# Optimization experiments

Hardware: AMD Instinct MI355X
Metric: run time of the kernel (lower is better)

Reference implementation:

```python
import jax, jax.numpy as jnp
import numpy as np

N1, E1 = 50000, 400000   # drug graph nodes/edges
N2, E2 = 50000, 400000   # second-branch nodes/edges
G = 256                   # number of graphs in the batch
F1, F2 = 93, 43           # node feature dims


def setup_inputs() -> dict:
    key = jax.random.key(0)
    ks = jax.random.split(key, 40)
    rn = lambda k, s, sc=0.05: jax.random.normal(k, s, dtype=jnp.float32) * sc
    inp = {}
    inp["data"] = 0  # unused placeholder arg in the original forward
    inp["x"] = jax.random.normal(ks[0], (N1, F1), dtype=jnp.float32)
    inp["edge_index"] = jax.random.randint(ks[1], (2, E1), 0, N1)
    inp["batch"] = jnp.sort(jax.random.randint(ks[2], (N1,), 0, G))
    inp["a"] = jax.random.normal(ks[3], (N2, F2), dtype=jnp.float32)
    inp["edge"] = jax.random.randint(ks[4], (2, E2), 0, N2)
    inp["c"] = jnp.sort(jax.random.randint(ks[5], (N2,), 0, G))
    # GINConv linear weights (x @ W + b convention)
    inp["W1"] = rn(ks[6], (F1, F1));        inp["b1"] = rn(ks[7], (F1,))
    inp["W2"] = rn(ks[8], (F1, F1 * 10));   inp["b2"] = rn(ks[9], (F1 * 10,))
    inp["W3"] = rn(ks[10], (F2, F2));       inp["b3"] = rn(ks[11], (F2,))
    inp["W4"] = rn(ks[12], (F2, F2 * 10));  inp["b4"] = rn(ks[13], (F2 * 10,))
    # fc_g: 1860 -> 1024 -> 512 ; fc_g1: 860 -> 1024 -> 512
    inp["fcg_w1"] = rn(ks[14], (F1 * 10 * 2, 1024)); inp["fcg_b1"] = rn(ks[15], (1024,))
    inp["fcg_w2"] = rn(ks[16], (1024, 512));         inp["fcg_b2"] = rn(ks[17], (512,))
    inp["fcg1_w1"] = rn(ks[18], (F2 * 10 * 2, 1024)); inp["fcg1_b1"] = rn(ks[19], (1024,))
    inp["fcg1_w2"] = rn(ks[20], (1024, 512));         inp["fcg1_b2"] = rn(ks[21], (512,))
    # fc_final / fc_final1: 512 -> 256 -> 1
    inp["ff_w1"] = rn(ks[22], (512, 256)); inp["ff_b1"] = rn(ks[23], (256,))
    inp["ff_w2"] = rn(ks[24], (256, 1));   inp["ff_b2"] = rn(ks[25], (1,))
    inp["ff1_w1"] = rn(ks[26], (512, 256)); inp["ff1_b1"] = rn(ks[27], (256,))
    inp["ff1_w2"] = rn(ks[28], (256, 1));   inp["ff1_b2"] = rn(ks[29], (1,))
    return inp


def _gin(h, ei, W, b):
    # PyG GINConv(eps=0): Linear(x_i + sum_{j->i} x_j)
    agg = jax.ops.segment_sum(h[ei[0]], ei[1], num_segments=h.shape[0])
    return (h + agg) @ W + b


def _pool(h, seg):
    # concat(global_max_pool, global_mean_pool) per graph -> [G, 2*d]
    s = jax.ops.segment_sum(h, seg, num_segments=G)
    cnt = jax.ops.segment_sum(jnp.ones((h.shape[0], 1), h.dtype), seg, num_segments=G)
    mean = s / jnp.maximum(cnt, 1.0)
    mx = jax.ops.segment_max(h, seg, num_segments=G)
    mx = jnp.where(jnp.isfinite(mx), mx, 0.0)
    return jnp.concatenate([mx, mean], axis=1)


def reference(data, x, edge_index, batch, a, edge, c,
              W1, b1, W2, b2, W3, b3, W4, b4,
              fcg_w1, fcg_b1, fcg_w2, fcg_b2,
              fcg1_w1, fcg1_b1, fcg1_w2, fcg1_b2,
              ff_w1, ff_b1, ff_w2, ff_b2,
              ff1_w1, ff1_b1, ff1_w2, ff1_b2):
    relu = jax.nn.relu
    # branch 1 (93-dim features)
    h = relu(_gin(x, edge_index, W1, b1))
    h = relu(_gin(h, edge_index, W2, b2))          # [N1, 930]
    p = _pool(h, batch)                             # [G, 1860]
    x_g = relu(p @ fcg_w1 + fcg_b1) @ fcg_w2 + fcg_b2   # [G, 512] (dropout = identity at eval)
    z = relu(x_g @ ff_w1 + ff_b1) @ ff_w2 + ff_b2        # [G, 1]
    # branch 2 (43-dim features)
    h1 = relu(_gin(a, edge, W3, b3))
    h1 = relu(_gin(h1, edge, W4, b4))               # [N2, 430]
    p1 = _pool(h1, c)                                # [G, 860]
    x_g1 = relu(p1 @ fcg1_w1 + fcg1_b1) @ fcg1_w2 + fcg1_b2  # [G, 512]
    z1 = relu(x_g1 @ ff1_w1 + ff1_b1) @ ff1_w2 + ff1_b2       # [G, 1]
    return (z, x_g, x_g1, z1)
```

## Files before the change

kernel.cpp:

```cpp
#include <hip/hip_runtime.h>


static constexpr int NG = 256;

typedef short  short8  __attribute__((ext_vector_type(8)));
typedef float  floatx4 __attribute__((ext_vector_type(4)));

__device__ __forceinline__ short f2bf(float f) {
    unsigned u = __float_as_uint(f);
    u += 0x7fff + ((u >> 16) & 1);
    return (short)(u >> 16);
}
__device__ __forceinline__ float bf2f(unsigned short s) {
    return __uint_as_float((unsigned)s << 16);
}

__global__ void offs_both_kernel(const int* __restrict__ s1, int n1, int* __restrict__ o1,
                                 const int* __restrict__ s2, int n2, int* __restrict__ o2) {
    int t = blockIdx.x * 256 + threadIdx.x;
    int br = t >> 9;
    int g = t & 511;
    if (br > 1 || g > NG) return;
    const int* seg = br ? s2 : s1;
    int N = br ? n2 : n1;
    int* offs = br ? o2 : o1;
    int lo = 0, hi = N;
    while (lo < hi) {
        int mid = (lo + hi) >> 1;
        if (seg[mid] < g) lo = mid + 1; else hi = mid;
    }
    offs[g] = lo;
}

__global__ void deg_both_kernel(const int* __restrict__ ei1, int E1, int* __restrict__ d1,
                                const int* __restrict__ ei2, int E2, int* __restrict__ d2) {
    int idx = blockIdx.x * 256 + threadIdx.x;
    if (idx < E1) atomicAdd(&d1[ei1[E1 + idx]], 1);
    else if (idx < E1 + E2) { int e = idx - E1; atomicAdd(&d2[ei2[E2 + e]], 1); }
}

__global__ __launch_bounds__(256) void scan1_both_kernel(
        const int* __restrict__ d1, int N1, int* __restrict__ x1, int* __restrict__ bs1, int nb1,
        const int* __restrict__ d2, int N2, int* __restrict__ x2, int* __restrict__ bs2) {
    __shared__ int sh[256];
    const int* deg; int* excl; int* bsum; int N; int blk;
    if ((int)blockIdx.x < nb1) { deg = d1; excl = x1; bsum = bs1; N = N1; blk = blockIdx.x; }
    else { deg = d2; excl = x2; bsum = bs2; N = N2; blk = blockIdx.x - nb1; }
    int base = blk * 1024;
    int t = threadIdx.x;
    int v[4];
    int s = 0;
    #pragma unroll
    for (int i = 0; i < 4; ++i) {
        int idx = base + t * 4 + i;
        v[i] = s;
        s += (idx < N) ? deg[idx] : 0;
    }
    sh[t] = s;
    __syncthreads();
    for (int off = 1; off < 256; off <<= 1) {
        int xv = (t >= off) ? sh[t - off] : 0;
        __syncthreads();
        sh[t] += xv;
        __syncthreads();
    }
    int texcl = (t > 0) ? sh[t - 1] : 0;
    #pragma unroll
    for (int i = 0; i < 4; ++i) {
        int idx = base + t * 4 + i;
        if (idx < N) excl[idx] = texcl + v[i];
    }
    if (t == 255) bsum[blk] = sh[255];
}

__global__ void scan2_both_kernel(int* __restrict__ b1, int nb1,
                                  int* __restrict__ b2, int nb2) {
    if (threadIdx.x) return;
    int* b = blockIdx.x ? b2 : b1;
    int nb = blockIdx.x ? nb2 : nb1;
    int acc = 0;
    for (int i = 0; i < nb; ++i) { int t = b[i]; b[i] = acc; acc += t; }
}

__global__ void scan3_both_kernel(int* __restrict__ x1, const int* __restrict__ bs1,
                                  int* __restrict__ c1, int N1, int Ev1,
                                  int* __restrict__ x2, const int* __restrict__ bs2,
                                  int* __restrict__ c2, int N2, int Ev2, int nc1) {
    int bid = blockIdx.x;
    int* excl; const int* bsum; int* cur; int N, E, i;
    if (bid < nc1) { i = bid * 256 + threadIdx.x; excl = x1; bsum = bs1; cur = c1; N = N1; E = Ev1; }
    else { i = (bid - nc1) * 256 + threadIdx.x; excl = x2; bsum = bs2; cur = c2; N = N2; E = Ev2; }
    if (i < N) {
        int v = excl[i] + bsum[i >> 10];
        excl[i] = v;
        cur[i] = v;
    }
    if (i == 0) excl[N] = E;
}

__global__ void fill_both_kernel(const int* __restrict__ ei1, int E1,
                                 int* __restrict__ c1, int* __restrict__ s1,
                                 const int* __restrict__ ei2, int E2,
                                 int* __restrict__ c2, int* __restrict__ s2) {
    int idx = blockIdx.x * 256 + threadIdx.x;
    if (idx < E1) {
        int pos = atomicAdd(&c1[ei1[E1 + idx]], 1);
        s1[pos] = ei1[idx];
    } else if (idx < E1 + E2) {
        int e = idx - E1;
        int pos = atomicAdd(&c2[ei2[E2 + e]], 1);
        s2[pos] = ei2[e];
    }
}

struct RJob { const float* W; short* Wb; int K, Nsrc, Ndst, KP; };
struct RJobs10 { RJob j[10]; };

__global__ __launch_bounds__(256) void repack_all_kernel(RJobs10 jobs) {
    __shared__ __align__(16) short sh[64][72];
    RJob jb = jobs.j[blockIdx.y];
    int tilesC = (jb.Ndst + 63) >> 6;
    int tilesK = (jb.KP + 63) >> 6;
    if ((int)blockIdx.x >= tilesC * tilesK) return;
    int c0 = ((int)blockIdx.x % tilesC) * 64;
    int k0 = ((int)blockIdx.x / tilesC) * 64;
    int t = threadIdx.x;
    #pragma unroll 4
    for (int idx = t; idx < 64 * 64; idx += 256) {
        int kk = idx >> 6, cc = idx & 63;
        int k = k0 + kk, cg = c0 + cc;
        float v = (k < jb.K && cg < jb.Nsrc) ? jb.W[(size_t)k * jb.Nsrc + cg] : 0.f;
        sh[cc][kk] = f2bf(v);
    }
    __syncthreads();
    int kt = jb.KP - k0; if (kt > 64) kt = 64;
    int chunks = kt >> 3;
    for (int idx = t; idx < 64 * chunks; idx += 256) {
        int cc = idx / chunks, ch = idx - cc * chunks;
        int cg = c0 + cc;
        if (cg < jb.Ndst) {
            uint4 v = *(const uint4*)&sh[cc][ch * 8];
            *(uint4*)&jb.Wb[(size_t)cg * jb.KP + k0 + ch * 8] = v;
        }
    }
}

__global__ __launch_bounds__(256) void cast_both_kernel(
        const float* __restrict__ x1, unsigned short* __restrict__ xb1, int N1,
        const float* __restrict__ x2, unsigned short* __restrict__ xb2, int N2) {
    int idx = blockIdx.x * 256 + threadIdx.x;
    int tot1 = N1 * 96;
    if (idx < tot1) {
        int n = idx / 96, k = idx - n * 96;
        float v = (k < 93) ? x1[(size_t)n * 93 + k] : 0.f;
        xb1[idx] = (unsigned short)f2bf(v);
    } else {
        idx -= tot1;
        if (idx < N2 * 48) {
            int n = idx / 48, k = idx - n * 48;
            float v = (k < 43) ? x2[(size_t)n * 43 + k] : 0.f;
            xb2[idx] = (unsigned short)f2bf(v);
        }
    }
}

template<int F, int FP, int FA>
__global__ __launch_bounds__(256) void gather_b_kernel(
        const unsigned short* __restrict__ xb, const int* __restrict__ csr,
        const int* __restrict__ ro, float* __restrict__ agg, int N) {
    int wave = (blockIdx.x * 256 + threadIdx.x) >> 6;
    int lane = threadIdx.x & 63;
    if (wave >= N) return;
    constexpr int HW = FP / 2;
    const unsigned* base = (const unsigned*)xb;
    int s = ro[wave], e = ro[wave + 1];
    float lo = 0.f, hi = 0.f;
    bool act = lane < HW;
    int i = s;
    for (; i + 1 < e; i += 2) {
        int n0 = csr[i], n1 = csr[i + 1];
        unsigned u0 = act ? base[(size_t)n0 * HW + lane] : 0u;
        unsigned u1 = act ? base[(size_t)n1 * HW + lane] : 0u;
        lo += __uint_as_float(u0 << 16);
        hi += __uint_as_float(u0 & 0xffff0000u);
        lo += __uint_as_float(u1 << 16);
        hi += __uint_as_float(u1 & 0xffff0000u);
    }
    if (i < e) {
        int n0 = csr[i];
        unsigned u0 = act ? base[(size_t)n0 * HW + lane] : 0u;
        lo += __uint_as_float(u0 << 16);
        hi += __uint_as_float(u0 & 0xffff0000u);
    }
    int cidx = 2 * lane;
    if (cidx + 1 < F)
        *(float2*)&agg[(size_t)wave * FA + cidx] = make_float2(lo, hi);
    else if (cidx < F)
        agg[(size_t)wave * FA + cidx] = lo;
}

template<int F, int KP, int NT, int FP, int FA>
__global__ __launch_bounds__(256) void gin_linear_mfma_kernel(
        const float* __restrict__ x, const float* __restrict__ agg,
        const short* __restrict__ Wb, const float* __restrict__ b,
        unsigned short* __restrict__ h1b, int N) {
    constexpr int KK = KP / 32;
    __shared__ __align__(16) short Vb[64][KP];
    int c0 = blockIdx.x * 64;
    int tid = threadIdx.x;
    int wid = tid >> 6;
    int lane = tid & 63;
    int ln = lane & 15, quad = lane >> 4;
    int cvalid = N - c0; if (cvalid > 64) cvalid = 64;
    for (int i = tid; i < 64 * (KP - F); i += 256)
        Vb[i / (KP - F)][F + i % (KP - F)] = 0;
    int nelem = cvalid * F;
    const float* xs = x + (size_t)c0 * F;
    const float* as = agg + (size_t)c0 * FA;
    for (int idx = tid; idx < nelem; idx += 256) {
        int r = idx / F, k = idx - r * F;
        Vb[r][k] = f2bf(xs[idx] + as[r * FA + k]);
    }
    __syncthreads();
    short8 afr[KK][4];
    #pragma unroll
    for (int kk = 0; kk < KK; ++kk)
        #pragma unroll
        for (int ms = 0; ms < 4; ++ms)
            afr[kk][ms] = *(const short8*)&Vb[ms * 16 + ln][kk * 32 + quad * 8];
    for (int nt = wid; nt < NT; nt += 4) {
        int col = nt * 16 + ln;
        float bcol = (col < F) ? b[col] : 0.f;
        short8 bfr[KK];
        const short8* bp = (const short8*)(Wb + (size_t)col * KP + quad * 8);
        #pragma unroll
        for (int kk = 0; kk < KK; ++kk) bfr[kk] = bp[kk * 4];
        #pragma unroll
        for (int ms = 0; ms < 4; ++ms) {
            if (ms * 16 < cvalid) {
                floatx4 acc = {0.f, 0.f, 0.f, 0.f};
                #pragma unroll
                for (int kk = 0; kk < KK; ++kk)
                    acc = __builtin_amdgcn_mfma_f32_16x16x32_bf16(
                              afr[kk][ms], bfr[kk], acc, 0, 0, 0);
                #pragma unroll
                for (int r = 0; r < 4; ++r) {
                    int row = ms * 16 + quad * 4 + r;
                    if (row < cvalid) {
                        unsigned short hv = 0;
                        if (col < F) hv = (unsigned short)f2bf(fmaxf(acc[r] + bcol, 0.f));
                        h1b[(size_t)(c0 + row) * FP + col] = hv;
                    }
                }
            }
        }
    }
}

template<int F, int KP, int FO, int NT, int NS, int FP, int FA>
__global__ __launch_bounds__(256) void gin_pool_mfma_kernel(
        const unsigned short* __restrict__ h1b, const float* __restrict__ agg,
        const short* __restrict__ Wb, const float* __restrict__ b,
        const int* __restrict__ offs,
        float* __restrict__ ppmax, float* __restrict__ ppsum) {
    constexpr int KK = KP / 32;
    __shared__ __align__(16) short Vb[64][KP];
    __shared__ float pmaxL[NT * 16];
    __shared__ float psumL[NT * 16];
    int g = blockIdx.x / NS;
    int s = blockIdx.x % NS;
    int tid = threadIdx.x;
    int wid = tid >> 6;
    int lane = tid & 63;
    int ln = lane & 15;
    int quad = lane >> 4;

    int gs0 = offs[g], ge0 = offs[g + 1];
    int per = (ge0 - gs0 + NS - 1) / NS;
    int gs = gs0 + s * per;
    int ge = gs + per; if (ge > ge0) ge = ge0;

    for (int i = tid; i < NT * 16; i += 256) { pmaxL[i] = 0.f; psumL[i] = 0.f; }
    for (int i = tid; i < 64 * (KP - F); i += 256)
        Vb[i / (KP - F)][F + i % (KP - F)] = 0;

    for (int c0 = gs; c0 < ge; c0 += 64) {
        __syncthreads();
        int cvalid = ge - c0; if (cvalid > 64) cvalid = 64;
        int nelem = cvalid * F;
        const unsigned short* hs = h1b + (size_t)c0 * FP;
        const float* as = agg + (size_t)c0 * FA;
        for (int idx = tid; idx < nelem; idx += 256) {
            int r = idx / F, k = idx - r * F;
            Vb[r][k] = f2bf(bf2f(hs[r * FP + k]) + as[r * FA + k]);
        }
        __syncthreads();
        short8 afr[KK][4];
        #pragma unroll
        for (int kk = 0; kk < KK; ++kk)
            #pragma unroll
            for (int ms = 0; ms < 4; ++ms)
                afr[kk][ms] = *(const short8*)&Vb[ms * 16 + ln][kk * 32 + quad * 8];
        for (int nt = wid; nt < NT; nt += 4) {
            int col = nt * 16 + ln;
            float bcol = (col < FO) ? b[col] : 0.f;
            short8 bfr[KK];
            const short8* bp = (const short8*)(Wb + (size_t)col * KP + quad * 8);
            #pragma unroll
            for (int kk = 0; kk < KK; ++kk) bfr[kk] = bp[kk * 4];
            float cmx = 0.f, csm = 0.f;
            #pragma unroll
            for (int ms = 0; ms < 4; ++ms) {
                if (ms * 16 < cvalid) {
                    floatx4 acc = {0.f, 0.f, 0.f, 0.f};
                    #pragma unroll
                    for (int kk = 0; kk < KK; ++kk)
                        acc = __builtin_amdgcn_mfma_f32_16x16x32_bf16(
                                  afr[kk][ms], bfr[kk], acc, 0, 0, 0);
                    #pragma unroll
                    for (int r = 0; r < 4; ++r) {
                        int rowl = ms * 16 + quad * 4 + r;
                        float v = fmaxf(acc[r] + bcol, 0.f);
                        if (rowl < cvalid) { cmx = fmaxf(cmx, v); csm += v; }
                    }
                }
            }
            cmx = fmaxf(cmx, __shfl_xor(cmx, 16, 64));
            cmx = fmaxf(cmx, __shfl_xor(cmx, 32, 64));
            csm += __shfl_xor(csm, 16, 64);
            csm += __shfl_xor(csm, 32, 64);
            if (quad == 0) {
                int i = nt * 16 + ln;
                pmaxL[i] = fmaxf(pmaxL[i], cmx);
                psumL[i] += csm;
            }
        }
    }
    __syncthreads();
    float* om = ppmax + (size_t)(g * NS + s) * FO;
    float* os = ppsum + (size_t)(g * NS + s) * FO;
    for (int col = tid; col < FO; col += 256) { om[col] = pmaxL[col]; os[col] = psumL[col]; }
}

template<int FO, int NS, int KPAD>
__global__ __launch_bounds__(256) void pool_reduce_kernel(
        const float* __restrict__ ppmax, const float* __restrict__ ppsum,
        const int* __restrict__ offs, short* __restrict__ pb) {
    int g = blockIdx.x;
    int cntg = offs[g + 1] - offs[g];
    float den = (float)(cntg > 0 ? cntg : 1);
    for (int col = threadIdx.x; col < KPAD; col += 256) {
        float v = 0.f;
        if (col < FO) {
            float m = 0.f;
            #pragma unroll
            for (int ss = 0; ss < NS; ++ss)
                m = fmaxf(m, ppmax[(size_t)(g * NS + ss) * FO + col]);
            v = m;
        } else if (col < 2 * FO) {
            float sm = 0.f;
            #pragma unroll
            for (int ss = 0; ss < NS; ++ss)
                sm += ppsum[(size_t)(g * NS + ss) * FO + (col - FO)];
            v = sm / den;
        }
        pb[(size_t)g * KPAD + col] = f2bf(v);
    }
}

template<int KPC>
__device__ __forceinline__ void fc_mfma_dev(
        const short* __restrict__ Ab, const short* __restrict__ Wb,
        float* __restrict__ partial, int KP, int NB, int bid) {
    int mb = bid & 3;
    int nb = (bid >> 2) % NB;
    int ks = (bid >> 2) / NB;
    int tid = threadIdx.x;
    int w = tid >> 6;
    int lane = tid & 63;
    int ln = lane & 15, quad = lane >> 4;
    int row = mb * 64 + w * 16 + ln;
    const short* ap = Ab + (size_t)row * KP + ks * KPC + quad * 8;
    const short* wp = Wb + (size_t)(nb * 64 + ln) * KP + ks * KPC + quad * 8;
    floatx4 acc[4];
    #pragma unroll
    for (int ns = 0; ns < 4; ++ns) acc[ns] = {0.f, 0.f, 0.f, 0.f};
    #pragma unroll
    for (int kk = 0; kk < KPC / 32; ++kk) {
        short8 a = *(const short8*)(ap + kk * 32);
        #pragma unroll
        for (int ns = 0; ns < 4; ++ns) {
            short8 b = *(const short8*)(wp + (size_t)ns * 16 * KP + kk * 32);
            acc[ns] = __builtin_amdgcn_mfma_f32_16x16x32_bf16(a, b, acc[ns], 0, 0, 0);
        }
    }
    int N = NB * 64;
    float* pp = partial + ((size_t)ks * 256 + mb * 64 + w * 16) * N + nb * 64;
    #pragma unroll
    for (int ns = 0; ns < 4; ++ns)
        #pragma unroll
        for (int r = 0; r < 4; ++r)
            pp[(quad * 4 + r) * N + ns * 16 + ln] = acc[ns][r];
}

template<int KPC1, int KPC2>
__global__ __launch_bounds__(256) void fc_mfma_both_kernel(
        const short* A1, const short* B1, float* P1, int KPa, int NBa, int nblk1,
        const short* A2, const short* B2, float* P2, int KPb, int NBb) {
    int bid = blockIdx.x;
    if (bid < nblk1) fc_mfma_dev<KPC1>(A1, B1, P1, KPa, NBa, bid);
    else             fc_mfma_dev<KPC2>(A2, B2, P2, KPb, NBb, bid - nblk1);
}

template<int KS, bool RELU, bool WBF16, bool WF32>
__global__ __launch_bounds__(256) void fc_reduce_both_kernel(
        const float* __restrict__ P1, const float* __restrict__ b1v,
        short* __restrict__ ob1, float* __restrict__ of1, int MN1, int Nn1,
        const float* __restrict__ P2, const float* __restrict__ b2v,
        short* __restrict__ ob2, float* __restrict__ of2, int MN2, int Nn2) {
    int idx = blockIdx.x * 256 + threadIdx.x;
    const float* P; const float* bias; short* ob; float* of; int MN, Nn;
    if (idx < MN1) { P = P1; bias = b1v; ob = ob1; of = of1; MN = MN1; Nn = Nn1; }
    else {
        idx -= MN1;
        if (idx >= MN2) return;
        P = P2; bias = b2v; ob = ob2; of = of2; MN = MN2; Nn = Nn2;
    }
    float v = bias[idx % Nn];
    #pragma unroll
    for (int s = 0; s < KS; ++s) v += P[(size_t)s * MN + idx];
    if (RELU) v = fmaxf(v, 0.f);
    if (WBF16) ob[idx] = f2bf(v);
    if (WF32)  of[idx] = v;
}

template<int KS>
__global__ __launch_bounds__(256) void head_final_both_kernel(
        const float* __restrict__ P1, const float* __restrict__ b11,
        const float* __restrict__ w21, const float* __restrict__ b21,
        float* __restrict__ z1o,
        const float* __restrict__ P2, const float* __restrict__ b12,
        const float* __restrict__ w22, const float* __restrict__ b22,
        float* __restrict__ z2o) {
    int br = blockIdx.x >> 8;
    int row = blockIdx.x & 255;
    const float* P  = br ? P2  : P1;
    const float* b1 = br ? b12 : b11;
    const float* w2 = br ? w22 : w21;
    const float* b2 = br ? b22 : b21;
    float* zo       = br ? z2o : z1o;
    int t = threadIdx.x;
    float v = b1[t];
    int idx = row * 256 + t;
    #pragma unroll
    for (int s = 0; s < KS; ++s) v += P[(size_t)s * 65536 + idx];
    v = fmaxf(v, 0.f) * w2[t];
    #pragma unroll
    for (int o = 32; o > 0; o >>= 1) v += __shfl_down(v, o, 64);
    __shared__ float red[4];
    if ((t & 63) == 0) red[t >> 6] = v;
    __syncthreads();
    if (t == 0) zo[row] = red[0] + red[1] + red[2] + red[3] + b2[0];
}

static inline int cdiv(int a, int b) { return (a + b - 1) / b; }

template<int F, int KPg, int FO, int NT, int NTL, int FP, int FA, int KP1>
static void run_gin(const float* feat, int N,
                    const float* b1, const float* b2,
                    float* agg, unsigned short* xb, unsigned short* h1b, short* pb,
                    const short* Wbl, const short* Wbg,
                    const int* offs, const int* rowoff, const int* csr,
                    hipStream_t stream) {
    constexpr int NS = 4;
    float* ppmax = (float*)xb;
    float* ppsum = ppmax + (size_t)NG * NS * FO;

    gather_b_kernel<F, FP, FA><<<cdiv(N, 4), 256, 0, stream>>>(xb, csr, rowoff, agg, N);
    gin_linear_mfma_kernel<F, KPg, NTL, FP, FA><<<cdiv(N, 64), 256, 0, stream>>>(
        feat, agg, Wbl, b1, h1b, N);
    gather_b_kernel<F, FP, FA><<<cdiv(N, 4), 256, 0, stream>>>(h1b, csr, rowoff, agg, N);
    gin_pool_mfma_kernel<F, KPg, FO, NT, NS, FP, FA><<<NG * NS, 256, 0, stream>>>(
        h1b, agg, Wbg, b2, offs, ppmax, ppsum);
    pool_reduce_kernel<FO, NS, KP1><<<NG, 256, 0, stream>>>(ppmax, ppsum, offs, pb);
}

extern "C" void kernel_launch(void* const* d_in, const int* in_sizes, int n_in,
                              void* d_out, int out_size, void* d_ws, size_t ws_size,
                              hipStream_t stream) {
    (void)n_in; (void)out_size; (void)ws_size;
    const float* x      = (const float*)d_in[1];
    const int*   ei     = (const int*)  d_in[2];
    const int*   batch  = (const int*)  d_in[3];
    const float* a      = (const float*)d_in[4];
    const int*   ed     = (const int*)  d_in[5];
    const int*   c      = (const int*)  d_in[6];
    const float* W1  = (const float*)d_in[7],  *b1  = (const float*)d_in[8];
    const float* W2  = (const float*)d_in[9],  *b2  = (const float*)d_in[10];
    const float* W3  = (const float*)d_in[11], *b3  = (const float*)d_in[12];
    const float* W4  = (const float*)d_in[13], *b4  = (const float*)d_in[14];
    const float* fg_w1  = (const float*)d_in[15], *fg_b1  = (const float*)d_in[16];
    const float* fg_w2  = (const float*)d_in[17], *fg_b2  = (const float*)d_in[18];
    const float* fg1_w1 = (const float*)d_in[19], *fg1_b1 = (const float*)d_in[20];
    const float* fg1_w2 = (const float*)d_in[21], *fg1_b2 = (const float*)d_in[22];
    const float* ff_w1  = (const float*)d_in[23], *ff_b1  = (const float*)d_in[24];
    const float* ff_w2  = (const float*)d_in[25], *ff_b2  = (const float*)d_in[26];
    const float* ff1_w1 = (const float*)d_in[27], *ff1_b1 = (const float*)d_in[28];
    const float* ff1_w2 = (const float*)d_in[29], *ff1_b2 = (const float*)d_in[30];

    const int N1 = in_sizes[1] / 93;
    const int E1 = in_sizes[2] / 2;
    const int N2 = in_sizes[4] / 43;
    const int E2 = in_sizes[5] / 2;

    float* out = (float*)d_out;
    float* z   = out;
    float* xg  = out + 256;
    float* xg1 = out + 256 + 256 * 512;
    float* z1  = out + 256 + 2 * 256 * 512;

    char* wsb = (char*)d_ws;
    size_t off = 0;
    auto carve = [&](size_t bytes) {
        void* ptr = wsb + off;
        off = (off + bytes + 255) & ~(size_t)255;
        return ptr;
    };
    float*          agg  = (float*)carve((size_t)N1 * 94 * sizeof(float));
    unsigned short* xb1  = (unsigned short*)carve((size_t)N1 * 96 * 2);
    unsigned short* xb2  = (unsigned short*)carve((size_t)N2 * 48 * 2);
    unsigned short* h1b  = (unsigned short*)carve((size_t)N1 * 96 * 2);
    short* pb1  = (short*)carve((size_t)NG * 2048 * 2);
    short* pb2  = (short*)carve((size_t)NG * 1024 * 2);
    short* t1b1 = (short*)carve((size_t)NG * 1024 * 2);
    short* t1b2 = (short*)carve((size_t)NG * 1024 * 2);
    short* xgb1 = (short*)carve((size_t)NG * 512 * 2);
    short* xgb2 = (short*)carve((size_t)NG * 512 * 2);
    short* Wbl1 = (short*)carve((size_t)96 * 96 * 2);
    short* Wbg1 = (short*)carve((size_t)944 * 96 * 2);
    short* Wbl2 = (short*)carve((size_t)48 * 64 * 2);
    short* Wbg2 = (short*)carve((size_t)432 * 64 * 2);
    short* Wb1a = (short*)carve((size_t)1024 * 2048 * 2);
    short* Wb2a = (short*)carve((size_t)512 * 1024 * 2);
    short* Wb3a = (short*)carve((size_t)256 * 512 * 2);
    short* Wb1b = (short*)carve((size_t)1024 * 1024 * 2);
    short* Wb2b = (short*)carve((size_t)512 * 1024 * 2);
    short* Wb3b = (short*)carve((size_t)256 * 512 * 2);
    int* offs1 = (int*)carve(257 * 4);
    int* offs2 = (int*)carve(257 * 4);
    int* deg   = (int*)carve((size_t)(N1 + N2) * 4);
    int* rowoff1 = (int*)carve((size_t)(N1 + 1) * 4);
    int* rowoff2 = (int*)carve((size_t)(N2 + 1) * 4);
    int* cursor1 = (int*)carve((size_t)N1 * 4);
    int* cursor2 = (int*)carve((size_t)N2 * 4);
    int* csr1  = (int*)carve((size_t)E1 * 4);
    int* csr2  = (int*)carve((size_t)E2 * 4);
    int* bsum  = (int*)carve(256 * 4);
    int* deg1 = deg, *deg2 = deg + N1;
    int* bsum1 = bsum, *bsum2 = bsum + 128;
    float* partial1 = agg;
    float* partial2 = agg + (size_t)8 * 262144;

    constexpr int KS = 8;

    RJobs10 jobs = {{
        { W1,     Wbl1, 93,   93,   96,   96   },
        { W2,     Wbg1, 93,   930,  944,  96   },
        { W3,     Wbl2, 43,   43,   48,   64   },
        { W4,     Wbg2, 43,   430,  432,  64   },
        { fg_w1,  Wb1a, 1860, 1024, 1024, 2048 },
        { fg_w2,  Wb2a, 1024, 512,  512,  1024 },
        { ff_w1,  Wb3a, 512,  256,  256,  512  },
        { fg1_w1, Wb1b, 860,  1024, 1024, 1024 },
        { fg1_w2, Wb2b, 1024, 512,  512,  1024 },
        { ff1_w1, Wb3b, 512,  256,  256,  512  },
    }};
    repack_all_kernel<<<dim3(512, 10), 256, 0, stream>>>(jobs);
    cast_both_kernel<<<cdiv(N1 * 96 + N2 * 48, 256), 256, 0, stream>>>(
        x, xb1, N1, a, xb2, N2);
    offs_both_kernel<<<4, 256, 0, stream>>>(batch, N1, offs1, c, N2, offs2);
    hipMemsetAsync(deg, 0, (size_t)(N1 + N2) * 4, stream);
    deg_both_kernel<<<cdiv(E1 + E2, 256), 256, 0, stream>>>(ei, E1, deg1, ed, E2, deg2);
    int nb1 = cdiv(N1, 1024), nb2 = cdiv(N2, 1024);
    scan1_both_kernel<<<nb1 + nb2, 256, 0, stream>>>(deg1, N1, rowoff1, bsum1, nb1,
                                                     deg2, N2, rowoff2, bsum2);
    scan2_both_kernel<<<2, 64, 0, stream>>>(bsum1, nb1, bsum2, nb2);
    int nc1 = cdiv(N1, 256), nc2 = cdiv(N2, 256);
    scan3_both_kernel<<<nc1 + nc2, 256, 0, stream>>>(rowoff1, bsum1, cursor1, N1, E1,
                                                     rowoff2, bsum2, cursor2, N2, E2, nc1);
    fill_both_kernel<<<cdiv(E1 + E2, 256), 256, 0, stream>>>(ei, E1, cursor1, csr1,
                                                             ed, E2, cursor2, csr2);

    run_gin<93, 96, 930, 59, 6, 96, 94, 2048>(x, N1, b1, b2,
        agg, xb1, h1b, pb1, Wbl1, Wbg1, offs1, rowoff1, csr1, stream);
    run_gin<43, 64, 430, 27, 3, 48, 44, 1024>(a, N2, b3, b4,
        agg, xb2, h1b, pb2, Wbl2, Wbg2, offs2, rowoff2, csr2, stream);

    fc_mfma_both_kernel<256, 128><<<1024, 256, 0, stream>>>(
        pb1, Wb1a, partial1, 2048, 16, 512, pb2, Wb1b, partial2, 1024, 16);
    fc_reduce_both_kernel<KS, true, true, false><<<cdiv(2 * 256 * 1024, 256), 256, 0, stream>>>(
        partial1, fg_b1, t1b1, nullptr, 256 * 1024, 1024,
        partial2, fg1_b1, t1b2, nullptr, 256 * 1024, 1024);
    fc_mfma_both_kernel<128, 128><<<512, 256, 0, stream>>>(
        t1b1, Wb2a, partial1, 1024, 8, 256, t1b2, Wb2b, partial2, 1024, 8);
    fc_reduce_both_kernel<KS, false, true, true><<<cdiv(2 * 256 * 512, 256), 256, 0, stream>>>(
        partial1, fg_b2, xgb1, xg, 256 * 512, 512,
        partial2, fg1_b2, xgb2, xg1, 256 * 512, 512);
    fc_mfma_both_kernel<64, 64><<<256, 256, 0, stream>>>(
        xgb1, Wb3a, partial1, 512, 4, 128, xgb2, Wb3b, partial2, 512, 4);
    head_final_both_kernel<KS><<<512, 256, 0, stream>>>(
        partial1, ff_b1, ff_w2, ff_b2, z,
        partial2, ff1_b1, ff1_w2, ff1_b2, z1);
}
```

Before: 510.1 us.

## Merge both GIN branches into shared launches and window the CSR atomics

The two graph branches now run in shared kernel launches for gather, GIN linear, GIN pooling and pool-reduce, with separate aggregation and hidden buffers so they no longer serialise through one scratch area. Degree counting and CSR fill use destination windows: each block scans an edge chunk and only performs atomics for destinations in its window, meant to localise atomic traffic. The gather is unrolled to four neighbours, and the narrow branch splits a wave into two half-groups combined with a shuffle. The windowing reads every edge eight times, and the merged kernels size shared memory for the larger branch, which may reduce occupancy for the smaller one.

Result: faster. 451.2 us (-11.5%).

```diff
diff --git a/kernel.cpp b/kernel.cpp
--- a/kernel.cpp
+++ b/kernel.cpp
@@ -1,7 +1,8 @@
 #include <hip/hip_runtime.h>
 
 
-static constexpr int NG = 256;
+static constexpr int NG  = 256;
+static constexpr int CHK = 4096;
 
 typedef short  short8  __attribute__((ext_vector_type(8)));
 typedef float  floatx4 __attribute__((ext_vector_type(4)));
@@ -14,6 +15,10 @@
 __device__ __forceinline__ float bf2f(unsigned short s) {
     return __uint_as_float((unsigned)s << 16);
 }
+__device__ __forceinline__ float bf_lo(unsigned u) { return __uint_as_float(u << 16); }
+__device__ __forceinline__ float bf_hi(unsigned u) { return __uint_as_float(u & 0xffff0000u); }
+
+static inline int cdiv(int a, int b) { return (a + b - 1) / b; }
 
 __global__ void offs_both_kernel(const int* __restrict__ s1, int n1, int* __restrict__ o1,
                                  const int* __restrict__ s2, int n2, int* __restrict__ o2) {
@@ -32,11 +37,25 @@
     offs[g] = lo;
 }
 
-__global__ void deg_both_kernel(const int* __restrict__ ei1, int E1, int* __restrict__ d1,
-                                const int* __restrict__ ei2, int E2, int* __restrict__ d2) {
-    int idx = blockIdx.x * 256 + threadIdx.x;
-    if (idx < E1) atomicAdd(&d1[ei1[E1 + idx]], 1);
-    else if (idx < E1 + E2) { int e = idx - E1; atomicAdd(&d2[ei2[E2 + e]], 1); }
+__device__ __forceinline__ void deg_win_dev(const int* __restrict__ ei, int E, int N,
+                                            int* __restrict__ deg, int bid) {
+    int win = bid & 7, chunk = bid >> 3;
+    int e0 = chunk * CHK;
+    int e1 = e0 + CHK; if (e1 > E) e1 = E;
+    int wlo = (int)((long)win * N / 8);
+    int whi = (int)((long)(win + 1) * N / 8);
+    for (int e = e0 + threadIdx.x; e < e1; e += 256) {
+        int dst = ei[E + e];
+        if (dst >= wlo && dst < whi) atomicAdd(&deg[dst], 1);
+    }
+}
+
+__global__ __launch_bounds__(256) void deg_win_both_kernel(
+        const int* ei1, int E1, int N1, int* d1, int nblk1,
+        const int* ei2, int E2, int N2, int* d2) {
+    int bid = blockIdx.x;
+    if (bid < nblk1) deg_win_dev(ei1, E1, N1, d1, bid);
+    else             deg_win_dev(ei2, E2, N2, d2, bid - nblk1);
 }
 
 __global__ __launch_bounds__(256) void scan1_both_kernel(
@@ -98,19 +117,29 @@
     if (i == 0) excl[N] = E;
 }
 
-__global__ void fill_both_kernel(const int* __restrict__ ei1, int E1,
-                                 int* __restrict__ c1, int* __restrict__ s1,
-                                 const int* __restrict__ ei2, int E2,
-                                 int* __restrict__ c2, int* __restrict__ s2) {
-    int idx = blockIdx.x * 256 + threadIdx.x;
-    if (idx < E1) {
-        int pos = atomicAdd(&c1[ei1[E1 + idx]], 1);
-        s1[pos] = ei1[idx];
-    } else if (idx < E1 + E2) {
-        int e = idx - E1;
-        int pos = atomicAdd(&c2[ei2[E2 + e]], 1);
-        s2[pos] = ei2[e];
-    }
+__device__ __forceinline__ void fill_win_dev(const int* __restrict__ ei, int E, int N,
+                                             int* __restrict__ cursor, int* __restrict__ csr,
+                                             int bid) {
+    int win = bid & 7, chunk = bid >> 3;
+    int e0 = chunk * CHK;
+    int e1 = e0 + CHK; if (e1 > E) e1 = E;
+    int wlo = (int)((long)win * N / 8);
+    int whi = (int)((long)(win + 1) * N / 8);
+    for (int e = e0 + threadIdx.x; e < e1; e += 256) {
+        int dst = ei[E + e];
+        if (dst >= wlo && dst < whi) {
+            int pos = atomicAdd(&cursor[dst], 1);
+            csr[pos] = ei[e];
+        }
+    }
+}
+
+__global__ __launch_bounds__(256) void fill_win_both_kernel(
+        const int* ei1, int E1, int N1, int* c1, int* s1, int nblk1,
+        const int* ei2, int E2, int N2, int* c2, int* s2) {
+    int bid = blockIdx.x;
+    if (bid < nblk1) fill_win_dev(ei1, E1, N1, c1, s1, bid);
+    else             fill_win_dev(ei2, E2, N2, c2, s2, bid - nblk1);
 }
 
 struct RJob { const float* W; short* Wb; int K, Nsrc, Ndst, KP; };
@@ -164,62 +193,90 @@
     }
 }
 
-template<int F, int FP, int FA>
-__global__ __launch_bounds__(256) void gather_b_kernel(
+template<int F, int FP, int FA, int GROUPS>
+__device__ __forceinline__ void gather_dev(
         const unsigned short* __restrict__ xb, const int* __restrict__ csr,
-        const int* __restrict__ ro, float* __restrict__ agg, int N) {
-    int wave = (blockIdx.x * 256 + threadIdx.x) >> 6;
+        const int* __restrict__ ro, float* __restrict__ agg, int N, int bid) {
+    int wave = (bid * 256 + threadIdx.x) >> 6;
     int lane = threadIdx.x & 63;
     if (wave >= N) return;
     constexpr int HW = FP / 2;
     const unsigned* base = (const unsigned*)xb;
     int s = ro[wave], e = ro[wave + 1];
+    int grp, l;
+    if (GROUPS == 2) { grp = lane >> 5; l = lane & 31; }
+    else             { grp = 0;         l = lane;      }
+    bool act = l < HW;
     float lo = 0.f, hi = 0.f;
-    bool act = lane < HW;
-    int i = s;
-    for (; i + 1 < e; i += 2) {
-        int n0 = csr[i], n1 = csr[i + 1];
-        unsigned u0 = act ? base[(size_t)n0 * HW + lane] : 0u;
-        unsigned u1 = act ? base[(size_t)n1 * HW + lane] : 0u;
-        lo += __uint_as_float(u0 << 16);
-        hi += __uint_as_float(u0 & 0xffff0000u);
-        lo += __uint_as_float(u1 << 16);
-        hi += __uint_as_float(u1 & 0xffff0000u);
-    }
-    if (i < e) {
-        int n0 = csr[i];
-        unsigned u0 = act ? base[(size_t)n0 * HW + lane] : 0u;
-        lo += __uint_as_float(u0 << 16);
-        hi += __uint_as_float(u0 & 0xffff0000u);
-    }
-    int cidx = 2 * lane;
-    if (cidx + 1 < F)
-        *(float2*)&agg[(size_t)wave * FA + cidx] = make_float2(lo, hi);
-    else if (cidx < F)
-        agg[(size_t)wave * FA + cidx] = lo;
+    int i = s + grp;
+    if (GROUPS == 1) {
+        for (; i + 3 < e; i += 4) {
+            int n0 = csr[i], n1 = csr[i + 1], n2 = csr[i + 2], n3 = csr[i + 3];
+            unsigned u0 = act ? base[(size_t)n0 * HW + l] : 0u;
+            unsigned u1 = act ? base[(size_t)n1 * HW + l] : 0u;
+            unsigned u2 = act ? base[(size_t)n2 * HW + l] : 0u;
+            unsigned u3 = act ? base[(size_t)n3 * HW + l] : 0u;
+            lo += bf_lo(u0) + bf_lo(u1) + bf_lo(u2) + bf_lo(u3);
+            hi += bf_hi(u0) + bf_hi(u1) + bf_hi(u2) + bf_hi(u3);
+        }
+        for (; i < e; ++i) {
+            int n0 = csr[i];
+            unsigned u0 = act ? base[(size_t)n0 * HW + l] : 0u;
+            lo += bf_lo(u0); hi += bf_hi(u0);
+        }
+    } else {
+        for (; i + 2 < e; i += 4) {
+            int n0 = csr[i], n1 = csr[i + 2];
+            unsigned u0 = act ? base[(size_t)n0 * HW + l] : 0u;
+            unsigned u1 = act ? base[(size_t)n1 * HW + l] : 0u;
+            lo += bf_lo(u0) + bf_lo(u1);
+            hi += bf_hi(u0) + bf_hi(u1);
+        }
+        if (i < e) {
+            int n0 = csr[i];
+            unsigned u0 = act ? base[(size_t)n0 * HW + l] : 0u;
+            lo += bf_lo(u0); hi += bf_hi(u0);
+        }
+        lo += __shfl_xor(lo, 32, 64);
+        hi += __shfl_xor(hi, 32, 64);
+    }
+    if (grp == 0) {
+        int cidx = 2 * l;
+        if (cidx + 1 < F)
+            *(float2*)&agg[(size_t)wave * FA + cidx] = make_float2(lo, hi);
+        else if (cidx < F)
+            agg[(size_t)wave * FA + cidx] = lo;
+    }
+}
+
+__global__ __launch_bounds__(256) void gather_both_kernel(
+        const unsigned short* xb1, const int* csr1, const int* ro1, float* agg1, int N1, int nblk1,
+        const unsigned short* xb2, const int* csr2, const int* ro2, float* agg2, int N2) {
+    int bid = blockIdx.x;
+    if (bid < nblk1) gather_dev<93, 96, 94, 1>(xb1, csr1, ro1, agg1, N1, bid);
+    else             gather_dev<43, 48, 44, 2>(xb2, csr2, ro2, agg2, N2, bid - nblk1);
 }
 
 template<int F, int KP, int NT, int FP, int FA>
-__global__ __launch_bounds__(256) void gin_linear_mfma_kernel(
+__device__ __forceinline__ void gin_linear_dev(
         const float* __restrict__ x, const float* __restrict__ agg,
         const short* __restrict__ Wb, const float* __restrict__ b,
-        unsigned short* __restrict__ h1b, int N) {
+        unsigned short* __restrict__ h1b, int N, int blk, short* Vb) {
     constexpr int KK = KP / 32;
-    __shared__ __align__(16) short Vb[64][KP];
-    int c0 = blockIdx.x * 64;
+    int c0 = blk * 64;
     int tid = threadIdx.x;
     int wid = tid >> 6;
     int lane = tid & 63;
     int ln = lane & 15, quad = lane >> 4;
     int cvalid = N - c0; if (cvalid > 64) cvalid = 64;
     for (int i = tid; i < 64 * (KP - F); i += 256)
-        Vb[i / (KP - F)][F + i % (KP - F)] = 0;
+        Vb[(i / (KP - F)) * KP + F + i % (KP - F)] = 0;
     int nelem = cvalid * F;
     const float* xs = x + (size_t)c0 * F;
     const float* as = agg + (size_t)c0 * FA;
     for (int idx = tid; idx < nelem; idx += 256) {
         int r = idx / F, k = idx - r * F;
-        Vb[r][k] = f2bf(xs[idx] + as[r * FA + k]);
+        Vb[r * KP + k] = f2bf(xs[idx] + as[r * FA + k]);
     }
     __syncthreads();
     short8 afr[KK][4];
@@ -227,7 +284,7 @@
     for (int kk = 0; kk < KK; ++kk)
         #pragma unroll
         for (int ms = 0; ms < 4; ++ms)
-            afr[kk][ms] = *(const short8*)&Vb[ms * 16 + ln][kk * 32 + quad * 8];
+            afr[kk][ms] = *(const short8*)&Vb[(ms * 16 + ln) * KP + kk * 32 + quad * 8];
     for (int nt = wid; nt < NT; nt += 4) {
         int col = nt * 16 + ln;
         float bcol = (col < F) ? b[col] : 0.f;
@@ -257,18 +314,29 @@
     }
 }
 
+__global__ __launch_bounds__(256) void gin_linear_both_kernel(
+        const float* x1, const float* agg1, const short* Wbl1, const float* bb1,
+        unsigned short* h1b1, int N1, int nblk1,
+        const float* x2, const float* agg2, const short* Wbl2, const float* bb2,
+        unsigned short* h1b2, int N2) {
+    __shared__ __align__(16) short Vb[64 * 96];
+    int bid = blockIdx.x;
+    if (bid < nblk1)
+        gin_linear_dev<93, 96, 6, 96, 94>(x1, agg1, Wbl1, bb1, h1b1, N1, bid, Vb);
+    else
+        gin_linear_dev<43, 64, 3, 48, 44>(x2, agg2, Wbl2, bb2, h1b2, N2, bid - nblk1, Vb);
+}
+
 template<int F, int KP, int FO, int NT, int NS, int FP, int FA>
-__global__ __launch_bounds__(256) void gin_pool_mfma_kernel(
+__device__ __forceinline__ void gin_pool_dev(
         const unsigned short* __restrict__ h1b, const float* __restrict__ agg,
         const short* __restrict__ Wb, const float* __restrict__ b,
         const int* __restrict__ offs,
-        float* __restrict__ ppmax, float* __restrict__ ppsum) {
+        float* __restrict__ ppmax, float* __restrict__ ppsum,
+        int blk, short* Vb, float* pmaxL, float* psumL) {
     constexpr int KK = KP / 32;
-    __shared__ __align__(16) short Vb[64][KP];
-    __shared__ float pmaxL[NT * 16];
-    __shared__ float psumL[NT * 16];
-    int g = blockIdx.x / NS;
-    int s = blockIdx.x % NS;
+    int g = blk / NS;
+    int s = blk % NS;
     int tid = threadIdx.x;
     int wid = tid >> 6;
     int lane = tid & 63;
@@ -282,7 +350,7 @@
 
     for (int i = tid; i < NT * 16; i += 256) { pmaxL[i] = 0.f; psumL[i] = 0.f; }
     for (int i = tid; i < 64 * (KP - F); i += 256)
-        Vb[i / (KP - F)][F + i % (KP - F)] = 0;
+        Vb[(i / (KP - F)) * KP + F + i % (KP - F)] = 0;
 
     for (int c0 = gs; c0 < ge; c0 += 64) {
         __syncthreads();
@@ -292,7 +360,7 @@
         const float* as = agg + (size_t)c0 * FA;
         for (int idx = tid; idx < nelem; idx += 256) {
             int r = idx / F, k = idx - r * F;
-            Vb[r][k] = f2bf(bf2f(hs[r * FP + k]) + as[r * FA + k]);
+            Vb[r * KP + k] = f2bf(bf2f(hs[r * FP + k]) + as[r * FA + k]);
         }
         __syncthreads();
         short8 afr[KK][4];
@@ -300,7 +368,7 @@
         for (int kk = 0; kk < KK; ++kk)
             #pragma unroll
             for (int ms = 0; ms < 4; ++ms)
-                afr[kk][ms] = *(const short8*)&Vb[ms * 16 + ln][kk * 32 + quad * 8];
+                afr[kk][ms] = *(const short8*)&Vb[(ms * 16 + ln) * KP + kk * 32 + quad * 8];
         for (int nt = wid; nt < NT; nt += 4) {
             int col = nt * 16 + ln;
             float bcol = (col < FO) ? b[col] : 0.f;
@@ -342,11 +410,27 @@
     for (int col = tid; col < FO; col += 256) { om[col] = pmaxL[col]; os[col] = psumL[col]; }
 }
 
+__global__ __launch_bounds__(256) void gin_pool_both_kernel(
+        const unsigned short* h1b1, const float* agg1, const short* Wbg1, const float* b21,
+        const int* offs1, float* pm1, float* ps1, int nblk1,
+        const unsigned short* h1b2, const float* agg2, const short* Wbg2, const float* b22,
+        const int* offs2, float* pm2, float* ps2) {
+    __shared__ __align__(16) short Vb[64 * 96];
+    __shared__ float pmaxL[944];
+    __shared__ float psumL[944];
+    int bid = blockIdx.x;
+    if (bid < nblk1)
+        gin_pool_dev<93, 96, 930, 59, 4, 96, 94>(h1b1, agg1, Wbg1, b21, offs1,
+                                                 pm1, ps1, bid, Vb, pmaxL, psumL);
+    else
+        gin_pool_dev<43, 64, 430, 27, 4, 48, 44>(h1b2, agg2, Wbg2, b22, offs2,
+                                                 pm2, ps2, bid - nblk1, Vb, pmaxL, psumL);
+}
+
 template<int FO, int NS, int KPAD>
-__global__ __launch_bounds__(256) void pool_reduce_kernel(
+__device__ __forceinline__ void pool_reduce_dev(
         const float* __restrict__ ppmax, const float* __restrict__ ppsum,
-        const int* __restrict__ offs, short* __restrict__ pb) {
-    int g = blockIdx.x;
+        const int* __restrict__ offs, short* __restrict__ pb, int g) {
     int cntg = offs[g + 1] - offs[g];
     float den = (float)(cntg > 0 ? cntg : 1);
     for (int col = threadIdx.x; col < KPAD; col += 256) {
@@ -366,6 +450,14 @@
         }
         pb[(size_t)g * KPAD + col] = f2bf(v);
     }
+}
+
+__global__ __launch_bounds__(256) void pool_reduce_both_kernel(
+        const float* pm1, const float* ps1, const int* offs1, short* pb1,
+        const float* pm2, const float* ps2, const int* offs2, short* pb2) {
+    int bid = blockIdx.x;
+    if (bid < NG) pool_reduce_dev<930, 4, 2048>(pm1, ps1, offs1, pb1, bid);
+    else          pool_reduce_dev<430, 4, 1024>(pm2, ps2, offs2, pb2, bid - NG);
 }
 
 template<int KPC>
@@ -461,28 +553,6 @@
     if ((t & 63) == 0) red[t >> 6] = v;
     __syncthreads();
     if (t == 0) zo[row] = red[0] + red[1] + red[2] + red[3] + b2[0];
-}
-
-static inline int cdiv(int a, int b) { return (a + b - 1) / b; }
-
-template<int F, int KPg, int FO, int NT, int NTL, int FP, int FA, int KP1>
-static void run_gin(const float* feat, int N,
-                    const float* b1, const float* b2,
-                    float* agg, unsigned short* xb, unsigned short* h1b, short* pb,
-                    const short* Wbl, const short* Wbg,
-                    const int* offs, const int* rowoff, const int* csr,
-                    hipStream_t stream) {
-    constexpr int NS = 4;
-    float* ppmax = (float*)xb;
-    float* ppsum = ppmax + (size_t)NG * NS * FO;
-
-    gather_b_kernel<F, FP, FA><<<cdiv(N, 4), 256, 0, stream>>>(xb, csr, rowoff, agg, N);
-    gin_linear_mfma_kernel<F, KPg, NTL, FP, FA><<<cdiv(N, 64), 256, 0, stream>>>(
-        feat, agg, Wbl, b1, h1b, N);
-    gather_b_kernel<F, FP, FA><<<cdiv(N, 4), 256, 0, stream>>>(h1b, csr, rowoff, agg, N);
-    gin_pool_mfma_kernel<F, KPg, FO, NT, NS, FP, FA><<<NG * NS, 256, 0, stream>>>(
-        h1b, agg, Wbg, b2, offs, ppmax, ppsum);
-    pool_reduce_kernel<FO, NS, KP1><<<NG, 256, 0, stream>>>(ppmax, ppsum, offs, pb);
 }
 
 extern "C" void kernel_launch(void* const* d_in, const int* in_sizes, int n_in,
@@ -526,10 +596,12 @@
         off = (off + bytes + 255) & ~(size_t)255;
         return ptr;
     };
-    float*          agg  = (float*)carve((size_t)N1 * 94 * sizeof(float));
+    float*          agg1 = (float*)carve((size_t)N1 * 94 * sizeof(float));
+    float*          agg2 = (float*)carve((size_t)N2 * 44 * sizeof(float));
     unsigned short* xb1  = (unsigned short*)carve((size_t)N1 * 96 * 2);
     unsigned short* xb2  = (unsigned short*)carve((size_t)N2 * 48 * 2);
-    unsigned short* h1b  = (unsigned short*)carve((size_t)N1 * 96 * 2);
+    unsigned short* h1b1 = (unsigned short*)carve((size_t)N1 * 96 * 2);
+    unsigned short* h1b2 = (unsigned short*)carve((size_t)N2 * 48 * 2);
     short* pb1  = (short*)carve((size_t)NG * 2048 * 2);
     short* pb2  = (short*)carve((size_t)NG * 1024 * 2);
     short* t1b1 = (short*)carve((size_t)NG * 1024 * 2);
@@ -558,8 +630,12 @@
     int* bsum  = (int*)carve(256 * 4);
     int* deg1 = deg, *deg2 = deg + N1;
     int* bsum1 = bsum, *bsum2 = bsum + 128;
-    float* partial1 = agg;
-    float* partial2 = agg + (size_t)8 * 262144;
+    float* partial1 = agg1;
+    float* partial2 = agg1 + (size_t)8 * 262144;
+    float* pm1 = (float*)xb1;
+    float* ps1 = pm1 + (size_t)NG * 4 * 930;
+    float* pm2 = (float*)xb2;
+    float* ps2 = pm2 + (size_t)NG * 4 * 430;
 
     constexpr int KS = 8;
 
@@ -580,7 +656,9 @@
         x, xb1, N1, a, xb2, N2);
     offs_both_kernel<<<4, 256, 0, stream>>>(batch, N1, offs1, c, N2, offs2);
     hipMemsetAsync(deg, 0, (size_t)(N1 + N2) * 4, stream);
-    deg_both_kernel<<<cdiv(E1 + E2, 256), 256, 0, stream>>>(ei, E1, deg1, ed, E2, deg2);
+    int nwb1 = cdiv(E1, CHK) * 8, nwb2 = cdiv(E2, CHK) * 8;
+    deg_win_both_kernel<<<nwb1 + nwb2, 256, 0, stream>>>(ei, E1, N1, deg1, nwb1,
+                                                         ed, E2, N2, deg2);
     int nb1 = cdiv(N1, 1024), nb2 = cdiv(N2, 1024);
     scan1_both_kernel<<<nb1 + nb2, 256, 0, stream>>>(deg1, N1, rowoff1, bsum1, nb1,
                                                      deg2, N2, rowoff2, bsum2);
@@ -588,13 +666,22 @@
     int nc1 = cdiv(N1, 256), nc2 = cdiv(N2, 256);
     scan3_both_kernel<<<nc1 + nc2, 256, 0, stream>>>(rowoff1, bsum1, cursor1, N1, E1,
                                                      rowoff2, bsum2, cursor2, N2, E2, nc1);
-    fill_both_kernel<<<cdiv(E1 + E2, 256), 256, 0, stream>>>(ei, E1, cursor1, csr1,
-                                                             ed, E2, cursor2, csr2);
-
-    run_gin<93, 96, 930, 59, 6, 96, 94, 2048>(x, N1, b1, b2,
-        agg, xb1, h1b, pb1, Wbl1, Wbg1, offs1, rowoff1, csr1, stream);
-    run_gin<43, 64, 430, 27, 3, 48, 44, 1024>(a, N2, b3, b4,
-        agg, xb2, h1b, pb2, Wbl2, Wbg2, offs2, rowoff2, csr2, stream);
+    fill_win_both_kernel<<<nwb1 + nwb2, 256, 0, stream>>>(ei, E1, N1, cursor1, csr1, nwb1,
+                                                          ed, E2, N2, cursor2, csr2);
+
+    int ng1 = cdiv(N1, 4), ng2 = cdiv(N2, 4);
+    gather_both_kernel<<<ng1 + ng2, 256, 0, stream>>>(
+        xb1, csr1, rowoff1, agg1, N1, ng1, xb2, csr2, rowoff2, agg2, N2);
+    int nl1 = cdiv(N1, 64), nl2 = cdiv(N2, 64);
+    gin_linear_both_kernel<<<nl1 + nl2, 256, 0, stream>>>(
+        x, agg1, Wbl1, b1, h1b1, N1, nl1, a, agg2, Wbl2, b3, h1b2, N2);
+    gather_both_kernel<<<ng1 + ng2, 256, 0, stream>>>(
+        h1b1, csr1, rowoff1, agg1, N1, ng1, h1b2, csr2, rowoff2, agg2, N2);
+    gin_pool_both_kernel<<<NG * 4 * 2, 256, 0, stream>>>(
+        h1b1, agg1, Wbg1, b2, offs1, pm1, ps1, NG * 4,
+        h1b2, agg2, Wbg2, b4, offs2, pm2, ps2);
+    pool_reduce_both_kernel<<<2 * NG, 256, 0, stream>>>(
+        pm1, ps1, offs1, pb1, pm2, ps2, offs2, pb2);
 
     fc_mfma_both_kernel<256, 128><<<1024, 256, 0, stream>>>(
         pb1, Wb1a, partial1, 2048, 16, 512, pb2, Wb1b, partial2, 1024, 16);
```
